# Optimization experiments

Measured on AMD Instinct MI355X. Metric: run time of the kernel, lower is better.

Reference implementation:

```python
import jax, jax.numpy as jnp
import numpy as np

CAUSAL = True


def setup_inputs() -> dict:
    key = jax.random.key(0)
    k1, k2, k3 = jax.random.split(key, 3)
    B, H, T, D = 2, 16, 2048, 64
    q = jax.random.normal(k1, (B, H, T, D), dtype=jnp.float32)
    k = jax.random.normal(k2, (B, H, T, D), dtype=jnp.float32)
    v = jax.random.normal(k3, (B, H, T, D), dtype=jnp.float32)
    return {"q": q, "k": k, "v": v}


def reference(q, k, v):
    # q,k,v: [B,H,T,D]
    d = q.shape[-1]
    scale = d ** -0.5
    dots = jnp.einsum('bhid,bhjd->bhij', q, k) * scale  # [B,H,T,T]
    if CAUSAL:
        t = q.shape[2]
        mask = jnp.triu(jnp.ones((t, t), dtype=bool), k=1)  # True above diagonal
        dots = jnp.where(mask, -jnp.inf, dots)
    attn = jax.nn.softmax(dots, axis=-1)
    # torch.einsum('bhjd,bhij->bhid', v, attn) == attn @ v
    return jnp.einsum('bhij,bhjd->bhid', attn, v)
```

## Files before the change

### kernel.cpp

```cpp
#include <hip/hip_runtime.h>
#include <hip/hip_bf16.h>

typedef unsigned short u16;
typedef unsigned int u32;
typedef __bf16 bf16x8 __attribute__((ext_vector_type(8)));
typedef short s16x4 __attribute__((ext_vector_type(4)));
typedef short s16x8 __attribute__((ext_vector_type(8)));
typedef float floatx4 __attribute__((ext_vector_type(4)));

#define T_SEQ 2048
#define HDIM 64
#define NBH 32

static __device__ __forceinline__ u16 f2b_rne(float x) {
    union { float f; u32 u; } c; c.f = x;
    u32 u = c.u;
    return (u16)((u + 0x7fffu + ((u >> 16) & 1u)) >> 16);
}
static __device__ __forceinline__ u16 f2b_trunc(float x) {
    union { float f; u32 u; } c; c.f = x;
    return (u16)(c.u >> 16);
}

#define GLOAD_LDS16(gp, lp)                                                      \
    __builtin_amdgcn_global_load_lds(                                            \
        (const __attribute__((address_space(1))) u32*)(gp),                      \
        (__attribute__((address_space(3))) u32*)(lp), 16, 0, 0)

__global__ __launch_bounds__(256) void prep(const float* __restrict__ k,
                                            const float* __restrict__ v,
                                            u16* __restrict__ kb,
                                            u16* __restrict__ vt) {
    __shared__ u16 tile[64][68];
    const int bh = blockIdx.y, t0 = blockIdx.x * 64;
    const int tid = threadIdx.x;

    const float* ksrc = k + ((size_t)bh * T_SEQ + t0) * HDIM;
    u16* kdst = kb + ((size_t)bh * T_SEQ + t0) * HDIM;
#pragma unroll
    for (int p = 0; p < 4; p++) {
        int idx = p * 256 + tid;
        float4 f = ((const float4*)ksrc)[idx];
        ushort4 o;
        o.x = f2b_rne(f.x); o.y = f2b_rne(f.y); o.z = f2b_rne(f.z); o.w = f2b_rne(f.w);
        ((ushort4*)kdst)[idx] = o;
    }

    const float* vsrc = v + ((size_t)bh * T_SEQ + t0) * HDIM;
#pragma unroll
    for (int p = 0; p < 4; p++) {
        int idx = p * 256 + tid;
        int r = idx >> 4, c4 = (idx & 15) * 4;
        float4 f = *(const float4*)(vsrc + r * HDIM + c4);
        tile[c4 + 0][r] = f2b_rne(f.x);
        tile[c4 + 1][r] = f2b_rne(f.y);
        tile[c4 + 2][r] = f2b_rne(f.z);
        tile[c4 + 3][r] = f2b_rne(f.w);
    }
    __syncthreads();
    u16* dst = vt + (size_t)bh * HDIM * T_SEQ + t0;
#pragma unroll
    for (int p = 0; p < 4; p++) {
        int idx = p * 256 + tid;
        int d = idx >> 4, c4 = (idx & 15) * 4;
        int t = c4 >> 4, qg = (c4 >> 2) & 3;
        int pos = qg * 16 + (t >> 1) * 8 + (t & 1) * 4;
        *(ushort4*)(dst + (size_t)d * T_SEQ + pos) = *(ushort4*)(&tile[d][c4]);
    }
}

__global__ __launch_bounds__(256, 4) void fattn(const float* __restrict__ q,
                                                const u16* __restrict__ kb,
                                                const u16* __restrict__ vtb,
                                                float* __restrict__ out) {
    __shared__ __align__(16) u16 Kl[2][64 * 64];
    __shared__ __align__(16) u16 Vl[2][64 * 64];

    const int bh = blockIdx.x;
    const int s = blockIdx.y;
    const int qt = (s & 8) ? (s ^ 7) : s;
    const int tid = threadIdx.x;
    const int wave = tid >> 6, lane = tid & 63;
    const int l15 = lane & 15, quad = lane >> 4;

    const float* qp = q + (size_t)bh * T_SEQ * HDIM;
    const u16* kp = kb + (size_t)bh * T_SEQ * HDIM;
    const u16* vp = vtb + (size_t)bh * HDIM * T_SEQ;

    const int qrow_base = qt * 64 + wave * 16;

    const int srow = wave * 8 + (lane >> 3);
    const int slot = lane & 7;
    const u16* kg0 = kp + srow * HDIM + (slot ^ (srow & 7)) * 8;
    const int vs = (slot - srow) & 7;
    const u16* vg0 = vp + (size_t)srow * T_SEQ + vs * 8;
    const u16* vg1 = vp + (size_t)(srow + 32) * T_SEQ + vs * 8;

    auto stage = [&](int j, int buf) {
        const u16* ks = kg0 + j * 64 * HDIM;
        u16* Kd = &Kl[buf][wave * 512];
        GLOAD_LDS16(ks, Kd);
        GLOAD_LDS16(ks + 32 * HDIM, Kd + 2048);
        u16* Vd = &Vl[buf][wave * 512];
        GLOAD_LDS16(vg0 + j * 64, Vd);
        GLOAD_LDS16(vg1 + j * 64, Vd + 2048);
    };

    stage(0, 0);

    const float SL2E = 0.125f * 1.44269504088896f;
    bf16x8 qf[2];
    {
        const float* qrow = qp + (size_t)(qrow_base + l15) * HDIM;
#pragma unroll
        for (int kc = 0; kc < 2; kc++) {
            const float4* p4 = (const float4*)(qrow + kc * 32 + quad * 8);
            float4 fa = p4[0], fb = p4[1];
            union { bf16x8 v; u16 s[8]; } cv;
            cv.s[0] = f2b_rne(fa.x * SL2E); cv.s[1] = f2b_rne(fa.y * SL2E);
            cv.s[2] = f2b_rne(fa.z * SL2E); cv.s[3] = f2b_rne(fa.w * SL2E);
            cv.s[4] = f2b_rne(fb.x * SL2E); cv.s[5] = f2b_rne(fb.y * SL2E);
            cv.s[6] = f2b_rne(fb.z * SL2E); cv.s[7] = f2b_rne(fb.w * SL2E);
            qf[kc] = cv.v;
        }
    }

    floatx4 o_acc[4];
#pragma unroll
    for (int dt = 0; dt < 4; dt++) o_acc[dt] = (floatx4){0.f, 0.f, 0.f, 0.f};
    float lsum = 0.f;

    for (int j = 0; j <= qt; ++j) {
        const int cur = j & 1;
        __syncthreads();

        if (j < qt) stage(j + 1, cur ^ 1);

        floatx4 sacc[4];
#pragma unroll
        for (int t = 0; t < 4; t++) sacc[t] = (floatx4){0.f, 0.f, 0.f, 0.f};
        const u16* Kc = Kl[cur];
#pragma unroll
        for (int kc = 0; kc < 2; kc++) {
#pragma unroll
            for (int t = 0; t < 4; t++) {
                int rk = t * 16 + l15;
                bf16x8 kf = *(const bf16x8*)(Kc + rk * 64 + ((kc * 4 + quad) ^ (rk & 7)) * 8);
                sacc[t] = __builtin_amdgcn_mfma_f32_16x16x32_bf16(kf, qf[kc], sacc[t], 0, 0, 0);
            }
        }

        s16x4 pfrag[4];
        const bool diag = (j == qt);
        const int gq = wave * 16 + l15;
#pragma unroll
        for (int t = 0; t < 4; t++) {
            union { s16x4 v; u16 h[4]; } pk;
#pragma unroll
            for (int rg = 0; rg < 4; rg++) {
                float e = __builtin_amdgcn_exp2f(sacc[t][rg]);
                if (diag && (t * 16 + quad * 4 + rg > gq)) e = 0.f;
                lsum += e;
                pk.h[rg] = f2b_trunc(e);
            }
            pfrag[t] = pk.v;
        }

        const u16* Vc = Vl[cur];
#pragma unroll
        for (int tp = 0; tp < 2; tp++) {
#pragma unroll
            for (int dt = 0; dt < 4; dt++) {
                int d = dt * 16 + l15;
                int sl = (quad * 2 + tp + d) & 7;
                s16x8 vf = *(const s16x8*)(Vc + d * 64 + sl * 8);
                s16x4 vf0 = __builtin_shufflevector(vf, vf, 0, 1, 2, 3);
                s16x4 vf1 = __builtin_shufflevector(vf, vf, 4, 5, 6, 7);
                o_acc[dt] = __builtin_amdgcn_mfma_f32_16x16x16bf16_1k(pfrag[2 * tp], vf0, o_acc[dt], 0, 0, 0);
                o_acc[dt] = __builtin_amdgcn_mfma_f32_16x16x16bf16_1k(pfrag[2 * tp + 1], vf1, o_acc[dt], 0, 0, 0);
            }
        }
    }

    float tot = lsum;
    tot += __shfl_xor(tot, 16, 64);
    tot += __shfl_xor(tot, 32, 64);
    float* op = out + (size_t)bh * T_SEQ * HDIM;
#pragma unroll
    for (int rg = 0; rg < 4; rg++) {
        float inv = 1.0f / __shfl(tot, quad * 4 + rg, 64);
        size_t row = (size_t)(qrow_base + quad * 4 + rg) * HDIM;
#pragma unroll
        for (int dt = 0; dt < 4; dt++)
            op[row + dt * 16 + l15] = o_acc[dt][rg] * inv;
    }
}

extern "C" void kernel_launch(void* const* d_in, const int* in_sizes, int n_in,
                              void* d_out, int out_size, void* d_ws, size_t ws_size,
                              hipStream_t stream) {
    const float* q = (const float*)d_in[0];
    const float* k = (const float*)d_in[1];
    const float* v = (const float*)d_in[2];
    float* out = (float*)d_out;

    u16* kb = (u16*)d_ws;
    u16* vt = kb + (size_t)NBH * T_SEQ * HDIM;

    prep<<<dim3(T_SEQ / 64, NBH), 256, 0, stream>>>(k, v, kb, vt);
    fattn<<<dim3(NBH, T_SEQ / 64), 256, 0, stream>>>(q, kb, vt, out);
}
```

Measured before the change: 123.5 us.

## Enlarge query tile to 128 rows per block, two 16-row fragments per wave

Each block now handles 128 query rows instead of 64, and each wave holds two 16-row Q fragments. Every K/V tile staged in LDS therefore feeds twice as many MFMAs, which halves K/V global loads and LDS staging per query row. Waves skip K tiles lying entirely above their causal diagonal, and the causal mask is applied only on tiles that straddle the diagonal. The grid halves to 16 query tiles per head with a new balanced ordering, and launch bounds drop to 2 blocks per CU to allow more registers, at the cost of fewer resident waves and coarser load balance.

After: 131.6 us. 6.5% more time.

```diff
diff --git a/kernel.cpp b/kernel.cpp
--- a/kernel.cpp
+++ b/kernel.cpp
@@ -69,7 +69,7 @@
     }
 }
 
-__global__ __launch_bounds__(256, 4) void fattn(const float* __restrict__ q,
+__global__ __launch_bounds__(256, 2) void fattn(const float* __restrict__ q,
                                                 const u16* __restrict__ kb,
                                                 const u16* __restrict__ vtb,
                                                 float* __restrict__ out) {
@@ -77,8 +77,8 @@
     __shared__ __align__(16) u16 Vl[2][64 * 64];
 
     const int bh = blockIdx.x;
-    const int s = blockIdx.y;
-    const int qt = (s & 8) ? (s ^ 7) : s;
+    const int sr = blockIdx.y;
+    const int st = (sr < 8) ? (2 * sr) : (2 * (15 - sr) + 1);
     const int tid = threadIdx.x;
     const int wave = tid >> 6, lane = tid & 63;
     const int l15 = lane & 15, quad = lane >> 4;
@@ -87,7 +87,8 @@
     const u16* kp = kb + (size_t)bh * T_SEQ * HDIM;
     const u16* vp = vtb + (size_t)bh * HDIM * T_SEQ;
 
-    const int qrow_base = qt * 64 + wave * 16;
+    const int iters = 2 * st + 2;
+    const int w32 = wave * 32;
 
     const int srow = wave * 8 + (lane >> 3);
     const int slot = lane & 7;
@@ -109,9 +110,10 @@
     stage(0, 0);
 
     const float SL2E = 0.125f * 1.44269504088896f;
-    bf16x8 qf[2];
-    {
-        const float* qrow = qp + (size_t)(qrow_base + l15) * HDIM;
+    bf16x8 qf[2][2];
+#pragma unroll
+    for (int qn = 0; qn < 2; qn++) {
+        const float* qrow = qp + (size_t)(st * 128 + w32 + qn * 16 + l15) * HDIM;
 #pragma unroll
         for (int kc = 0; kc < 2; kc++) {
             const float4* p4 = (const float4*)(qrow + kc * 32 + quad * 8);
@@ -121,78 +123,109 @@
             cv.s[2] = f2b_rne(fa.z * SL2E); cv.s[3] = f2b_rne(fa.w * SL2E);
             cv.s[4] = f2b_rne(fb.x * SL2E); cv.s[5] = f2b_rne(fb.y * SL2E);
             cv.s[6] = f2b_rne(fb.z * SL2E); cv.s[7] = f2b_rne(fb.w * SL2E);
-            qf[kc] = cv.v;
+            qf[qn][kc] = cv.v;
         }
     }
 
-    floatx4 o_acc[4];
-#pragma unroll
-    for (int dt = 0; dt < 4; dt++) o_acc[dt] = (floatx4){0.f, 0.f, 0.f, 0.f};
-    float lsum = 0.f;
-
-    for (int j = 0; j <= qt; ++j) {
+    floatx4 o_acc[2][4];
+#pragma unroll
+    for (int qn = 0; qn < 2; qn++)
+#pragma unroll
+        for (int dt = 0; dt < 4; dt++) o_acc[qn][dt] = (floatx4){0.f, 0.f, 0.f, 0.f};
+    float lsum[2] = {0.f, 0.f};
+
+    for (int j = 0; j < iters; ++j) {
         const int cur = j & 1;
         __syncthreads();
 
-        if (j < qt) stage(j + 1, cur ^ 1);
-
-        floatx4 sacc[4];
-#pragma unroll
-        for (int t = 0; t < 4; t++) sacc[t] = (floatx4){0.f, 0.f, 0.f, 0.f};
-        const u16* Kc = Kl[cur];
-#pragma unroll
-        for (int kc = 0; kc < 2; kc++) {
-#pragma unroll
-            for (int t = 0; t < 4; t++) {
-                int rk = t * 16 + l15;
-                bf16x8 kf = *(const bf16x8*)(Kc + rk * 64 + ((kc * 4 + quad) ^ (rk & 7)) * 8);
-                sacc[t] = __builtin_amdgcn_mfma_f32_16x16x32_bf16(kf, qf[kc], sacc[t], 0, 0, 0);
+        if (j + 1 < iters) stage(j + 1, cur ^ 1);
+
+        const int rel = j * 64 - st * 128;
+        if (rel <= w32 + 31) {
+            floatx4 sacc[2][4];
+#pragma unroll
+            for (int qn = 0; qn < 2; qn++)
+#pragma unroll
+                for (int kt = 0; kt < 4; kt++) sacc[qn][kt] = (floatx4){0.f, 0.f, 0.f, 0.f};
+            const u16* Kc = Kl[cur];
+#pragma unroll
+            for (int kc = 0; kc < 2; kc++) {
+#pragma unroll
+                for (int kt = 0; kt < 4; kt++) {
+                    int rk = kt * 16 + l15;
+                    bf16x8 kf = *(const bf16x8*)(Kc + rk * 64 + ((kc * 4 + quad) ^ (rk & 7)) * 8);
+                    sacc[0][kt] = __builtin_amdgcn_mfma_f32_16x16x32_bf16(kf, qf[0][kc], sacc[0][kt], 0, 0, 0);
+                    sacc[1][kt] = __builtin_amdgcn_mfma_f32_16x16x32_bf16(kf, qf[1][kc], sacc[1][kt], 0, 0, 0);
+                }
+            }
+
+            s16x4 pfrag[2][4];
+            if (rel + 63 >= w32) {
+#pragma unroll
+                for (int qn = 0; qn < 2; qn++) {
+                    const int gq = w32 + qn * 16 + l15;
+#pragma unroll
+                    for (int kt = 0; kt < 4; kt++) {
+                        union { s16x4 v; u16 h[4]; } pk;
+#pragma unroll
+                        for (int rg = 0; rg < 4; rg++) {
+                            float e = __builtin_amdgcn_exp2f(sacc[qn][kt][rg]);
+                            if (rel + kt * 16 + quad * 4 + rg > gq) e = 0.f;
+                            lsum[qn] += e;
+                            pk.h[rg] = f2b_trunc(e);
+                        }
+                        pfrag[qn][kt] = pk.v;
+                    }
+                }
+            } else {
+#pragma unroll
+                for (int qn = 0; qn < 2; qn++)
+#pragma unroll
+                    for (int kt = 0; kt < 4; kt++) {
+                        union { s16x4 v; u16 h[4]; } pk;
+#pragma unroll
+                        for (int rg = 0; rg < 4; rg++) {
+                            float e = __builtin_amdgcn_exp2f(sacc[qn][kt][rg]);
+                            lsum[qn] += e;
+                            pk.h[rg] = f2b_trunc(e);
+                        }
+                        pfrag[qn][kt] = pk.v;
+                    }
+            }
+
+            const u16* Vc = Vl[cur];
+#pragma unroll
+            for (int tp = 0; tp < 2; tp++) {
+#pragma unroll
+                for (int dt = 0; dt < 4; dt++) {
+                    int d = dt * 16 + l15;
+                    int sl = (quad * 2 + tp + d) & 7;
+                    s16x8 vf = *(const s16x8*)(Vc + d * 64 + sl * 8);
+                    s16x4 vf0 = __builtin_shufflevector(vf, vf, 0, 1, 2, 3);
+                    s16x4 vf1 = __builtin_shufflevector(vf, vf, 4, 5, 6, 7);
+                    o_acc[0][dt] = __builtin_amdgcn_mfma_f32_16x16x16bf16_1k(pfrag[0][2 * tp], vf0, o_acc[0][dt], 0, 0, 0);
+                    o_acc[0][dt] = __builtin_amdgcn_mfma_f32_16x16x16bf16_1k(pfrag[0][2 * tp + 1], vf1, o_acc[0][dt], 0, 0, 0);
+                    o_acc[1][dt] = __builtin_amdgcn_mfma_f32_16x16x16bf16_1k(pfrag[1][2 * tp], vf0, o_acc[1][dt], 0, 0, 0);
+                    o_acc[1][dt] = __builtin_amdgcn_mfma_f32_16x16x16bf16_1k(pfrag[1][2 * tp + 1], vf1, o_acc[1][dt], 0, 0, 0);
+                }
             }
         }
-
-        s16x4 pfrag[4];
-        const bool diag = (j == qt);
-        const int gq = wave * 16 + l15;
-#pragma unroll
-        for (int t = 0; t < 4; t++) {
-            union { s16x4 v; u16 h[4]; } pk;
-#pragma unroll
-            for (int rg = 0; rg < 4; rg++) {
-                float e = __builtin_amdgcn_exp2f(sacc[t][rg]);
-                if (diag && (t * 16 + quad * 4 + rg > gq)) e = 0.f;
-                lsum += e;
-                pk.h[rg] = f2b_trunc(e);
-            }
-            pfrag[t] = pk.v;
+    }
+
+    float* op = out + (size_t)bh * T_SEQ * HDIM;
+#pragma unroll
+    for (int qn = 0; qn < 2; qn++) {
+        float tot = lsum[qn];
+        tot += __shfl_xor(tot, 16, 64);
+        tot += __shfl_xor(tot, 32, 64);
+#pragma unroll
+        for (int rg = 0; rg < 4; rg++) {
+            float inv = 1.0f / __shfl(tot, quad * 4 + rg, 64);
+            size_t row = (size_t)(st * 128 + w32 + qn * 16 + quad * 4 + rg) * HDIM;
+#pragma unroll
+            for (int dt = 0; dt < 4; dt++)
+                op[row + dt * 16 + l15] = o_acc[qn][dt][rg] * inv;
         }
-
-        const u16* Vc = Vl[cur];
-#pragma unroll
-        for (int tp = 0; tp < 2; tp++) {
-#pragma unroll
-            for (int dt = 0; dt < 4; dt++) {
-                int d = dt * 16 + l15;
-                int sl = (quad * 2 + tp + d) & 7;
-                s16x8 vf = *(const s16x8*)(Vc + d * 64 + sl * 8);
-                s16x4 vf0 = __builtin_shufflevector(vf, vf, 0, 1, 2, 3);
-                s16x4 vf1 = __builtin_shufflevector(vf, vf, 4, 5, 6, 7);
-                o_acc[dt] = __builtin_amdgcn_mfma_f32_16x16x16bf16_1k(pfrag[2 * tp], vf0, o_acc[dt], 0, 0, 0);
-                o_acc[dt] = __builtin_amdgcn_mfma_f32_16x16x16bf16_1k(pfrag[2 * tp + 1], vf1, o_acc[dt], 0, 0, 0);
-            }
-        }
-    }
-
-    float tot = lsum;
-    tot += __shfl_xor(tot, 16, 64);
-    tot += __shfl_xor(tot, 32, 64);
-    float* op = out + (size_t)bh * T_SEQ * HDIM;
-#pragma unroll
-    for (int rg = 0; rg < 4; rg++) {
-        float inv = 1.0f / __shfl(tot, quad * 4 + rg, 64);
-        size_t row = (size_t)(qrow_base + quad * 4 + rg) * HDIM;
-#pragma unroll
-        for (int dt = 0; dt < 4; dt++)
-            op[row + dt * 16 + l15] = o_acc[dt][rg] * inv;
     }
 }
 
@@ -208,5 +241,5 @@
     u16* vt = kb + (size_t)NBH * T_SEQ * HDIM;
 
     prep<<<dim3(T_SEQ / 64, NBH), 256, 0, stream>>>(k, v, kb, vt);
-    fattn<<<dim3(NBH, T_SEQ / 64), 256, 0, stream>>>(q, kb, vt, out);
-}
+    fattn<<<dim3(NBH, 16), 256, 0, stream>>>(q, kb, vt, out);
+}
```
